# Performance work log

Measured on AMD Instinct MI355X. Metric: run time of the kernel, lower is better.

Reference implementation:

```python
import jax, jax.numpy as jnp
import numpy as np

N_NODES = 100000
N_EDGES = 1600000
D = 128        # in_dim == hidden_dim (forced by x_j + xe in message)
C = 64         # num_classes
G = 128        # number of graphs in the batch
BN_EPS = 1e-5


def setup_inputs() -> dict:
    key = jax.random.key(0)
    ks = jax.random.split(key, 14)
    s = 0.05
    inp = {
        "x": jax.random.normal(ks[0], (N_NODES, D), dtype=jnp.float32),
        "xe": jax.random.normal(ks[1], (N_EDGES, D), dtype=jnp.float32),
        "edge_index": jax.random.randint(ks[2], (2, N_EDGES), 0, N_NODES, dtype=jnp.int32),
        "batch": jnp.sort(jax.random.randint(ks[3], (N_NODES,), 0, G, dtype=jnp.int32)),
        # layer 0 MySAGEConv params
        "Wl0": jax.random.normal(ks[4], (D, D), dtype=jnp.float32) * s,
        "bl0": jnp.zeros((D,), dtype=jnp.float32),
        "Wr0": jax.random.normal(ks[5], (D, D), dtype=jnp.float32) * s,
        # layer 1 MySAGEConv params
        "Wl1": jax.random.normal(ks[6], (D, D), dtype=jnp.float32) * s,
        "bl1": jnp.zeros((D,), dtype=jnp.float32),
        "Wr1": jax.random.normal(ks[7], (D, D), dtype=jnp.float32) * s,
        # BatchNorm (only applied after non-final layers -> layer 0)
        "gamma0": jnp.ones((D,), dtype=jnp.float32),
        "beta0": jnp.zeros((D,), dtype=jnp.float32),
        # readout projection
        "Wp": jax.random.normal(ks[8], (C, D), dtype=jnp.float32) * s,
        "bp": jnp.zeros((C,), dtype=jnp.float32),
    }
    return inp


def _segment_mean(vals, idx, num_segments):
    s = jax.ops.segment_sum(vals, idx, num_segments=num_segments)
    cnt = jax.ops.segment_sum(jnp.ones((vals.shape[0],), vals.dtype), idx,
                              num_segments=num_segments)
    return s / jnp.clip(cnt, 1.0)[:, None]


def _my_sage_conv(h, xe, src, dst, Wl, bl, Wr):
    # message: relu(x_j + xe); aggregate: scatter-mean at dst; then lin_l + lin_r
    msg = jax.nn.relu(h[src] + xe)                       # [E, D]
    agg = _segment_mean(msg, dst, N_NODES)               # [N, D]
    return agg @ Wl.T + bl + h @ Wr.T


def _batchnorm_train(h, gamma, beta):
    mu = jnp.mean(h, axis=0)
    var = jnp.var(h, axis=0)
    return gamma * (h - mu) * jax.lax.rsqrt(var + BN_EPS) + beta


def reference(x, xe, edge_index, batch,
              Wl0, bl0, Wr0, Wl1, bl1, Wr1,
              gamma0, beta0, Wp, bp):
    src, dst = edge_index[0], edge_index[1]
    # layer 0: conv -> BN -> ReLU
    h = _my_sage_conv(x, xe, src, dst, Wl0, bl0, Wr0)
    h = jax.nn.relu(_batchnorm_train(h, gamma0, beta0))
    # layer 1 (last): conv only
    h = _my_sage_conv(h, xe, src, dst, Wl1, bl1, Wr1)
    # graph readout (global mean pool over pre-proj node features)
    g = _segment_mean(h, batch, G)                       # [G, D]
    # readout projection on nodes
    h = jax.nn.relu(h) @ Wp.T + bp                       # [N, C]
    return h, g
```

## Files before the change

kernel.cpp:

```cpp
#include <hip/hip_runtime.h>

#define N_NODES 100000
#define N_EDGES 1600000
#define DIM 128
#define NCLS 64
#define NG 128
#define BN_EPS 1e-5f

typedef __attribute__((ext_vector_type(8))) short s16x8;
typedef __attribute__((ext_vector_type(4))) float f32x4;
#define MFMA_BF16 __builtin_amdgcn_mfma_f32_16x16x32_bf16

__device__ __forceinline__ void f2hl8(float4 v0, float4 v1, s16x8& h8, s16x8& l8) {
    float vv[8] = {v0.x, v0.y, v0.z, v0.w, v1.x, v1.y, v1.z, v1.w};
#pragma unroll
    for (int i = 0; i < 8; ++i) {
        unsigned u = __float_as_uint(vv[i]);
        short h = (short)(u >> 16);
        float r = vv[i] - __uint_as_float(u & 0xFFFF0000u);
        short l = (short)(__float_as_uint(r) >> 16);
        h8[i] = h;
        l8[i] = l;
    }
}

__device__ __forceinline__ float4 relu4(float4 v) {
    v.x = fmaxf(v.x, 0.f); v.y = fmaxf(v.y, 0.f);
    v.z = fmaxf(v.z, 0.f); v.w = fmaxf(v.w, 0.f);
    return v;
}

__global__ void k_hist(const int* __restrict__ dst, int* __restrict__ cnt) {
    int e = blockIdx.x * 256 + threadIdx.x;
    if (e < N_EDGES) atomicAdd(&cnt[dst[e]], 1);
}

__global__ void k_scan1(const int* __restrict__ cnt, int* __restrict__ rowptr,
                        int* __restrict__ bsums) {
    __shared__ int sd[1024];
    int tid = threadIdx.x;
    int i = blockIdx.x * 1024 + tid;
    int v = (i < N_NODES) ? cnt[i] : 0;
    sd[tid] = v;
    __syncthreads();
    for (int off = 1; off < 1024; off <<= 1) {
        int t2 = (tid >= off) ? sd[tid - off] : 0;
        __syncthreads();
        sd[tid] += t2;
        __syncthreads();
    }
    if (i < N_NODES) rowptr[i] = sd[tid] - v;
    if (tid == 1023) bsums[blockIdx.x] = sd[tid];
}

__global__ void k_scan2(int* __restrict__ bsums, int nb) {
    __shared__ int sd[128];
    int t = threadIdx.x;
    int v = (t < nb) ? bsums[t] : 0;
    sd[t] = v;
    __syncthreads();
    for (int off = 1; off < 128; off <<= 1) {
        int u = (t >= off) ? sd[t - off] : 0;
        __syncthreads();
        sd[t] += u;
        __syncthreads();
    }
    if (t < nb) bsums[t] = sd[t] - v;
}

__global__ void k_scan3(int* __restrict__ rowptr, const int* __restrict__ bsums,
                        int* __restrict__ wcur) {
    int i = blockIdx.x * 1024 + threadIdx.x;
    if (i < N_NODES) {
        int v = rowptr[i] + bsums[blockIdx.x];
        rowptr[i] = v;
        wcur[i] = v;
    }
    if (i == N_NODES - 1) rowptr[N_NODES] = N_EDGES;
}

__global__ void k_scatter(const int* __restrict__ src, const int* __restrict__ dst,
                          int* __restrict__ wcur, int2* __restrict__ esort) {
    int e = blockIdx.x * 256 + threadIdx.x;
    if (e < N_EDGES) {
        int d = dst[e];
        int p = atomicAdd(&wcur[d], 1);
        esort[p] = make_int2(e, src[e]);
    }
}

__global__ __launch_bounds__(256) void k_agg(
        const float* __restrict__ F, const float* __restrict__ xe,
        const int* __restrict__ rowptr, const int2* __restrict__ esort,
        float* __restrict__ agg, const float* __restrict__ bnsc, int applyBN) {
    int wid = (blockIdx.x * blockDim.x + threadIdx.x) >> 6;
    int lane = threadIdx.x & 63;
    if (wid >= N_NODES) return;
    int half = lane >> 5;
    int l = lane & 31;
    int p0 = rowptr[wid], p1 = rowptr[wid + 1];
    if (p0 == p1) {
        if (half == 0) {
            float4 z = make_float4(0.f, 0.f, 0.f, 0.f);
            *reinterpret_cast<float4*>(&agg[(size_t)wid * DIM + l * 4]) = z;
        }
        return;
    }
    float4 sc, sh;
    if (applyBN) {
        sc = *reinterpret_cast<const float4*>(&bnsc[l * 4]);
        sh = *reinterpret_cast<const float4*>(&bnsc[DIM + l * 4]);
    }
    float4 acc = make_float4(0.f, 0.f, 0.f, 0.f);
    for (int p = p0; p < p1; p += 8) {
        int q0 = p + half;
        int q1 = p + 2 + half;
        int q2 = p + 4 + half;
        int q3 = p + 6 + half;
        int2 e0 = esort[min(q0, p1 - 1)];
        int2 e1 = esort[min(q1, p1 - 1)];
        int2 e2 = esort[min(q2, p1 - 1)];
        int2 e3 = esort[min(q3, p1 - 1)];
        float4 a0 = *reinterpret_cast<const float4*>(&F[(size_t)e0.y * DIM + l * 4]);
        float4 b0 = *reinterpret_cast<const float4*>(&xe[(size_t)e0.x * DIM + l * 4]);
        float4 a1 = *reinterpret_cast<const float4*>(&F[(size_t)e1.y * DIM + l * 4]);
        float4 b1 = *reinterpret_cast<const float4*>(&xe[(size_t)e1.x * DIM + l * 4]);
        float4 a2 = *reinterpret_cast<const float4*>(&F[(size_t)e2.y * DIM + l * 4]);
        float4 b2 = *reinterpret_cast<const float4*>(&xe[(size_t)e2.x * DIM + l * 4]);
        float4 a3 = *reinterpret_cast<const float4*>(&F[(size_t)e3.y * DIM + l * 4]);
        float4 b3 = *reinterpret_cast<const float4*>(&xe[(size_t)e3.x * DIM + l * 4]);
        if (applyBN) {
            a0.x = fmaxf(a0.x * sc.x + sh.x, 0.f); a0.y = fmaxf(a0.y * sc.y + sh.y, 0.f);
            a0.z = fmaxf(a0.z * sc.z + sh.z, 0.f); a0.w = fmaxf(a0.w * sc.w + sh.w, 0.f);
            a1.x = fmaxf(a1.x * sc.x + sh.x, 0.f); a1.y = fmaxf(a1.y * sc.y + sh.y, 0.f);
            a1.z = fmaxf(a1.z * sc.z + sh.z, 0.f); a1.w = fmaxf(a1.w * sc.w + sh.w, 0.f);
            a2.x = fmaxf(a2.x * sc.x + sh.x, 0.f); a2.y = fmaxf(a2.y * sc.y + sh.y, 0.f);
            a2.z = fmaxf(a2.z * sc.z + sh.z, 0.f); a2.w = fmaxf(a2.w * sc.w + sh.w, 0.f);
            a3.x = fmaxf(a3.x * sc.x + sh.x, 0.f); a3.y = fmaxf(a3.y * sc.y + sh.y, 0.f);
            a3.z = fmaxf(a3.z * sc.z + sh.z, 0.f); a3.w = fmaxf(a3.w * sc.w + sh.w, 0.f);
        }
        if (q0 < p1) {
            acc.x += fmaxf(a0.x + b0.x, 0.f); acc.y += fmaxf(a0.y + b0.y, 0.f);
            acc.z += fmaxf(a0.z + b0.z, 0.f); acc.w += fmaxf(a0.w + b0.w, 0.f);
        }
        if (q1 < p1) {
            acc.x += fmaxf(a1.x + b1.x, 0.f); acc.y += fmaxf(a1.y + b1.y, 0.f);
            acc.z += fmaxf(a1.z + b1.z, 0.f); acc.w += fmaxf(a1.w + b1.w, 0.f);
        }
        if (q2 < p1) {
            acc.x += fmaxf(a2.x + b2.x, 0.f); acc.y += fmaxf(a2.y + b2.y, 0.f);
            acc.z += fmaxf(a2.z + b2.z, 0.f); acc.w += fmaxf(a2.w + b2.w, 0.f);
        }
        if (q3 < p1) {
            acc.x += fmaxf(a3.x + b3.x, 0.f); acc.y += fmaxf(a3.y + b3.y, 0.f);
            acc.z += fmaxf(a3.z + b3.z, 0.f); acc.w += fmaxf(a3.w + b3.w, 0.f);
        }
    }
    acc.x += __shfl_xor(acc.x, 32);
    acc.y += __shfl_xor(acc.y, 32);
    acc.z += __shfl_xor(acc.z, 32);
    acc.w += __shfl_xor(acc.w, 32);
    if (half == 0) {
        float s = 1.f / (float)(p1 - p0);
        acc.x *= s; acc.y *= s; acc.z *= s; acc.w *= s;
        *reinterpret_cast<float4*>(&agg[(size_t)wid * DIM + l * 4]) = acc;
    }
}

__global__ void k_wprep_all(const float* __restrict__ Wl0, const float* __restrict__ Wr0,
                            const float* __restrict__ Wl1, const float* __restrict__ Wr1,
                            const float* __restrict__ Wp,
                            short* __restrict__ fWl0h, short* __restrict__ fWl0l,
                            short* __restrict__ fWr0h, short* __restrict__ fWr0l,
                            short* __restrict__ fWl1h, short* __restrict__ fWl1l,
                            short* __restrict__ fWr1h, short* __restrict__ fWr1l,
                            short* __restrict__ fWph, short* __restrict__ fWpl) {
    int b = blockIdx.x;
    const float* W; short* hi; short* lo; int ct;
    if (b < 8)       { W = Wl0; hi = fWl0h; lo = fWl0l; ct = b; }
    else if (b < 16) { W = Wr0; hi = fWr0h; lo = fWr0l; ct = b - 8; }
    else if (b < 24) { W = Wl1; hi = fWl1h; lo = fWl1l; ct = b - 16; }
    else if (b < 32) { W = Wr1; hi = fWr1h; lo = fWr1l; ct = b - 24; }
    else             { W = Wp;  hi = fWph;  lo = fWpl;  ct = b - 32; }
    int tt = threadIdx.x;
    int lane = tt & 63, ks = (tt >> 6) & 3;
    int row = ct * 16 + (lane & 15);
    int k0 = ks * 32 + ((lane >> 4) << 3);
    float4 v0 = *reinterpret_cast<const float4*>(&W[(size_t)row * DIM + k0]);
    float4 v1 = *reinterpret_cast<const float4*>(&W[(size_t)row * DIM + k0 + 4]);
    s16x8 h8, l8;
    f2hl8(v0, v1, h8, l8);
    int t = ct * 256 + ks * 64 + lane;
    *reinterpret_cast<s16x8*>(&hi[(size_t)t * 8]) = h8;
    *reinterpret_cast<s16x8*>(&lo[(size_t)t * 8]) = l8;
}

__global__ __launch_bounds__(256) void k_gemm2(
        const float* __restrict__ A, const float* __restrict__ B,
        const short* __restrict__ fW1h, const short* __restrict__ fW1l,
        const short* __restrict__ fW2h, const short* __restrict__ fW2l,
        const float* __restrict__ bias, float* __restrict__ OUT,
        float* __restrict__ bnacc, const float* __restrict__ bnsc,
        int doBN, int bnB) {
    int t = threadIdx.x, w = t >> 6, l = t & 63;
    int n0 = blockIdx.x * 128;
    int r = l & 15, kh = l >> 4;
    int row0 = n0 + w * 16 + r;
    int row1 = row0 + 64;
    int n_0 = min(row0, N_NODES - 1);
    int n_1 = min(row1, N_NODES - 1);

    f32x4 acc0[8], acc1[8];
#pragma unroll
    for (int ct = 0; ct < 8; ++ct) {
        acc0[ct] = (f32x4){0.f, 0.f, 0.f, 0.f};
        acc1[ct] = (f32x4){0.f, 0.f, 0.f, 0.f};
    }
    const s16x8* w1h = (const s16x8*)fW1h;
    const s16x8* w1l = (const s16x8*)fW1l;
    const s16x8* w2h = (const s16x8*)fW2h;
    const s16x8* w2l = (const s16x8*)fW2l;

#pragma unroll
    for (int ks = 0; ks < 4; ++ks) {
        int kb = ks * 32 + kh * 8;
        float4 va0 = *reinterpret_cast<const float4*>(&A[(size_t)n_0 * DIM + kb]);
        float4 va1 = *reinterpret_cast<const float4*>(&A[(size_t)n_0 * DIM + kb + 4]);
        float4 vb0 = *reinterpret_cast<const float4*>(&B[(size_t)n_0 * DIM + kb]);
        float4 vb1 = *reinterpret_cast<const float4*>(&B[(size_t)n_0 * DIM + kb + 4]);
        float4 wa0 = *reinterpret_cast<const float4*>(&A[(size_t)n_1 * DIM + kb]);
        float4 wa1 = *reinterpret_cast<const float4*>(&A[(size_t)n_1 * DIM + kb + 4]);
        float4 wb0 = *reinterpret_cast<const float4*>(&B[(size_t)n_1 * DIM + kb]);
        float4 wb1 = *reinterpret_cast<const float4*>(&B[(size_t)n_1 * DIM + kb + 4]);
        if (bnB) {
            float4 sc0 = *reinterpret_cast<const float4*>(&bnsc[kb]);
            float4 sh0 = *reinterpret_cast<const float4*>(&bnsc[DIM + kb]);
            float4 sc1 = *reinterpret_cast<const float4*>(&bnsc[kb + 4]);
            float4 sh1 = *reinterpret_cast<const float4*>(&bnsc[DIM + kb + 4]);
            vb0.x = fmaxf(vb0.x * sc0.x + sh0.x, 0.f);
            vb0.y = fmaxf(vb0.y * sc0.y + sh0.y, 0.f);
            vb0.z = fmaxf(vb0.z * sc0.z + sh0.z, 0.f);
            vb0.w = fmaxf(vb0.w * sc0.w + sh0.w, 0.f);
            vb1.x = fmaxf(vb1.x * sc1.x + sh1.x, 0.f);
            vb1.y = fmaxf(vb1.y * sc1.y + sh1.y, 0.f);
            vb1.z = fmaxf(vb1.z * sc1.z + sh1.z, 0.f);
            vb1.w = fmaxf(vb1.w * sc1.w + sh1.w, 0.f);
            wb0.x = fmaxf(wb0.x * sc0.x + sh0.x, 0.f);
            wb0.y = fmaxf(wb0.y * sc0.y + sh0.y, 0.f);
            wb0.z = fmaxf(wb0.z * sc0.z + sh0.z, 0.f);
            wb0.w = fmaxf(wb0.w * sc0.w + sh0.w, 0.f);
            wb1.x = fmaxf(wb1.x * sc1.x + sh1.x, 0.f);
            wb1.y = fmaxf(wb1.y * sc1.y + sh1.y, 0.f);
            wb1.z = fmaxf(wb1.z * sc1.z + sh1.z, 0.f);
            wb1.w = fmaxf(wb1.w * sc1.w + sh1.w, 0.f);
        }
        s16x8 a0h, a0l, b0h, b0l, a1h, a1l, b1h, b1l;
        f2hl8(va0, va1, a0h, a0l);
        f2hl8(vb0, vb1, b0h, b0l);
        f2hl8(wa0, wa1, a1h, a1l);
        f2hl8(wb0, wb1, b1h, b1l);
        int fb = ks * 64 + l;
#pragma unroll
        for (int ct = 0; ct < 8; ++ct) {
            int fi = ct * 256 + fb;
            s16x8 wh1 = w1h[fi], wl1 = w1l[fi];
            s16x8 wh2 = w2h[fi], wl2 = w2l[fi];
            acc0[ct] = MFMA_BF16(a0h, wh1, acc0[ct], 0, 0, 0);
            acc0[ct] = MFMA_BF16(a0h, wl1, acc0[ct], 0, 0, 0);
            acc0[ct] = MFMA_BF16(a0l, wh1, acc0[ct], 0, 0, 0);
            acc0[ct] = MFMA_BF16(b0h, wh2, acc0[ct], 0, 0, 0);
            acc0[ct] = MFMA_BF16(b0h, wl2, acc0[ct], 0, 0, 0);
            acc0[ct] = MFMA_BF16(b0l, wh2, acc0[ct], 0, 0, 0);
            acc1[ct] = MFMA_BF16(a1h, wh1, acc1[ct], 0, 0, 0);
            acc1[ct] = MFMA_BF16(a1h, wl1, acc1[ct], 0, 0, 0);
            acc1[ct] = MFMA_BF16(a1l, wh1, acc1[ct], 0, 0, 0);
            acc1[ct] = MFMA_BF16(b1h, wh2, acc1[ct], 0, 0, 0);
            acc1[ct] = MFMA_BF16(b1h, wl2, acc1[ct], 0, 0, 0);
            acc1[ct] = MFMA_BF16(b1l, wh2, acc1[ct], 0, 0, 0);
        }
    }

    float p1s[8], p2s[8];
    int col0 = l & 15;
    int nb0 = n0 + w * 16 + (kh << 2);
    int nb1 = nb0 + 64;
#pragma unroll
    for (int ct = 0; ct < 8; ++ct) {
        float bj = bias[ct * 16 + col0];
        float s1 = 0.f, s2 = 0.f;
#pragma unroll
        for (int rr = 0; rr < 4; ++rr) {
            int n = nb0 + rr;
            float h = acc0[ct][rr] + bj;
            if (n < N_NODES) {
                OUT[(size_t)n * DIM + ct * 16 + col0] = h;
                s1 += h; s2 += h * h;
            }
            n = nb1 + rr;
            h = acc1[ct][rr] + bj;
            if (n < N_NODES) {
                OUT[(size_t)n * DIM + ct * 16 + col0] = h;
                s1 += h; s2 += h * h;
            }
        }
        p1s[ct] = s1; p2s[ct] = s2;
    }
    if (doBN) {
        __shared__ float red1[512];
        __shared__ float red2[512];
#pragma unroll
        for (int ct = 0; ct < 8; ++ct) {
            p1s[ct] += __shfl_xor(p1s[ct], 16);
            p1s[ct] += __shfl_xor(p1s[ct], 32);
            p2s[ct] += __shfl_xor(p2s[ct], 16);
            p2s[ct] += __shfl_xor(p2s[ct], 32);
        }
        if (l < 16) {
#pragma unroll
            for (int ct = 0; ct < 8; ++ct) {
                red1[w * 128 + ct * 16 + l] = p1s[ct];
                red2[w * 128 + ct * 16 + l] = p2s[ct];
            }
        }
        __syncthreads();
        if (t < 128) {
            float s1 = red1[t] + red1[128 + t] + red1[256 + t] + red1[384 + t];
            float s2 = red2[t] + red2[128 + t] + red2[256 + t] + red2[384 + t];
            atomicAdd(&bnacc[t], s1);
            atomicAdd(&bnacc[128 + t], s2);
        }
    }
}

__global__ void k_bnfinal(const float* __restrict__ bnacc, const float* __restrict__ gamma,
                          const float* __restrict__ beta, float* __restrict__ bnsc) {
    int d = threadIdx.x;
    if (d < DIM) {
        float mu = bnacc[d] / (float)N_NODES;
        float var = bnacc[128 + d] / (float)N_NODES - mu * mu;
        float rstd = rsqrtf(var + BN_EPS);
        float sc = gamma[d] * rstd;
        bnsc[d] = sc;
        bnsc[128 + d] = beta[d] - mu * sc;
    }
}

__global__ void k_pool(const float* __restrict__ H1, const int* __restrict__ batch,
                       float* __restrict__ gout) {
    __shared__ float red[4][128];
    int g = blockIdx.x;
    int t = threadIdx.x;
    int d = t & 127;
    int sl = t >> 7;
    int lo = 0, hi = N_NODES;
    while (lo < hi) { int m = (lo + hi) >> 1; if (batch[m] < g) lo = m + 1; else hi = m; }
    int s = lo;
    lo = 0; hi = N_NODES;
    while (lo < hi) { int m = (lo + hi) >> 1; if (batch[m] < g + 1) lo = m + 1; else hi = m; }
    int e = lo;
    float sum = 0.f;
    for (int n = s + sl; n < e; n += 4) sum += H1[(size_t)n * DIM + d];
    red[sl][d] = sum;
    __syncthreads();
    if (t < 128) {
        float tot = red[0][d] + red[1][d] + red[2][d] + red[3][d];
        gout[g * DIM + d] = tot / (float)max(e - s, 1);
    }
}

__global__ __launch_bounds__(256) void k_proj(
        const float* __restrict__ H1, const short* __restrict__ fWph,
        const short* __restrict__ fWpl, const float* __restrict__ bp,
        float* __restrict__ OUT) {
    int t = threadIdx.x, w = t >> 6, l = t & 63;
    int n0 = blockIdx.x * 128;
    int r = l & 15, kh = l >> 4;
    int row0 = n0 + w * 16 + r;
    int row1 = row0 + 64;
    int n_0 = min(row0, N_NODES - 1);
    int n_1 = min(row1, N_NODES - 1);
    f32x4 acc0[4], acc1[4];
#pragma unroll
    for (int ct = 0; ct < 4; ++ct) {
        acc0[ct] = (f32x4){0.f, 0.f, 0.f, 0.f};
        acc1[ct] = (f32x4){0.f, 0.f, 0.f, 0.f};
    }
    const s16x8* wph = (const s16x8*)fWph;
    const s16x8* wpl = (const s16x8*)fWpl;
#pragma unroll
    for (int ks = 0; ks < 4; ++ks) {
        int kb = ks * 32 + kh * 8;
        float4 va0 = relu4(*reinterpret_cast<const float4*>(&H1[(size_t)n_0 * DIM + kb]));
        float4 va1 = relu4(*reinterpret_cast<const float4*>(&H1[(size_t)n_0 * DIM + kb + 4]));
        float4 wa0 = relu4(*reinterpret_cast<const float4*>(&H1[(size_t)n_1 * DIM + kb]));
        float4 wa1 = relu4(*reinterpret_cast<const float4*>(&H1[(size_t)n_1 * DIM + kb + 4]));
        s16x8 a0h, a0l, a1h, a1l;
        f2hl8(va0, va1, a0h, a0l);
        f2hl8(wa0, wa1, a1h, a1l);
        int fb = ks * 64 + l;
#pragma unroll
        for (int ct = 0; ct < 4; ++ct) {
            int fi = ct * 256 + fb;
            s16x8 wh = wph[fi], wl = wpl[fi];
            acc0[ct] = MFMA_BF16(a0h, wh, acc0[ct], 0, 0, 0);
            acc0[ct] = MFMA_BF16(a0h, wl, acc0[ct], 0, 0, 0);
            acc0[ct] = MFMA_BF16(a0l, wh, acc0[ct], 0, 0, 0);
            acc1[ct] = MFMA_BF16(a1h, wh, acc1[ct], 0, 0, 0);
            acc1[ct] = MFMA_BF16(a1h, wl, acc1[ct], 0, 0, 0);
            acc1[ct] = MFMA_BF16(a1l, wh, acc1[ct], 0, 0, 0);
        }
    }
    int col0 = l & 15;
    int nb0 = n0 + w * 16 + (kh << 2);
    int nb1 = nb0 + 64;
#pragma unroll
    for (int ct = 0; ct < 4; ++ct) {
        float bj = bp[ct * 16 + col0];
#pragma unroll
        for (int rr = 0; rr < 4; ++rr) {
            int n = nb0 + rr;
            if (n < N_NODES)
                OUT[(size_t)n * NCLS + ct * 16 + col0] = acc0[ct][rr] + bj;
            n = nb1 + rr;
            if (n < N_NODES)
                OUT[(size_t)n * NCLS + ct * 16 + col0] = acc1[ct][rr] + bj;
        }
    }
}

extern "C" void kernel_launch(void* const* d_in, const int* in_sizes, int n_in,
                              void* d_out, int out_size, void* d_ws, size_t ws_size,
                              hipStream_t stream) {
    (void)in_sizes; (void)n_in; (void)out_size; (void)ws_size;
    const float* x     = (const float*)d_in[0];
    const float* xe    = (const float*)d_in[1];
    const int*   eidx  = (const int*)d_in[2];
    const int*   batch = (const int*)d_in[3];
    const float* Wl0   = (const float*)d_in[4];
    const float* bl0   = (const float*)d_in[5];
    const float* Wr0   = (const float*)d_in[6];
    const float* Wl1   = (const float*)d_in[7];
    const float* bl1   = (const float*)d_in[8];
    const float* Wr1   = (const float*)d_in[9];
    const float* gamma0 = (const float*)d_in[10];
    const float* beta0  = (const float*)d_in[11];
    const float* Wp    = (const float*)d_in[12];
    const float* bp    = (const float*)d_in[13];
    const int* srcp = eidx;
    const int* dstp = eidx + N_EDGES;

    char* ws = (char*)d_ws;
    size_t off = 0;
    auto carve = [&](size_t bytes) {
        void* p = ws + off;
        off = (off + bytes + 255) & ~(size_t)255;
        return p;
    };
    int*   cnt    = (int*)carve((size_t)N_NODES * 4);
    int*   rowptr = (int*)carve((size_t)(N_NODES + 1) * 4);
    int*   wcur   = (int*)carve((size_t)N_NODES * 4);
    int*   bsums  = (int*)carve(128 * 4);
    float* bnacc  = (float*)carve(256 * 4);
    float* bnsc   = (float*)carve(256 * 4);
    int2*  esort  = (int2*)carve((size_t)N_EDGES * 8);
    float* AGG    = (float*)carve((size_t)N_NODES * DIM * 4);
    float* H      = (float*)carve((size_t)N_NODES * DIM * 4);
    float* H1     = (float*)carve((size_t)N_NODES * DIM * 4);
    short* fWl0h = (short*)carve(16384 * 2);
    short* fWl0l = (short*)carve(16384 * 2);
    short* fWr0h = (short*)carve(16384 * 2);
    short* fWr0l = (short*)carve(16384 * 2);
    short* fWl1h = (short*)carve(16384 * 2);
    short* fWl1l = (short*)carve(16384 * 2);
    short* fWr1h = (short*)carve(16384 * 2);
    short* fWr1l = (short*)carve(16384 * 2);
    short* fWph  = (short*)carve(8192 * 2);
    short* fWpl  = (short*)carve(8192 * 2);

    float* out_h = (float*)d_out;
    float* out_g = out_h + (size_t)N_NODES * NCLS;

    hipMemsetAsync(cnt, 0, (size_t)N_NODES * 4, stream);
    hipMemsetAsync(bnacc, 0, 256 * 4, stream);

    k_wprep_all<<<36, 256, 0, stream>>>(Wl0, Wr0, Wl1, Wr1, Wp,
                                        fWl0h, fWl0l, fWr0h, fWr0l,
                                        fWl1h, fWl1l, fWr1h, fWr1l,
                                        fWph, fWpl);

    int nb = (N_NODES + 1023) / 1024;
    k_hist<<<(N_EDGES + 255) / 256, 256, 0, stream>>>(dstp, cnt);
    k_scan1<<<nb, 1024, 0, stream>>>(cnt, rowptr, bsums);
    k_scan2<<<1, 128, 0, stream>>>(bsums, nb);
    k_scan3<<<nb, 1024, 0, stream>>>(rowptr, bsums, wcur);
    k_scatter<<<(N_EDGES + 255) / 256, 256, 0, stream>>>(srcp, dstp, wcur, esort);

    int gblocks = (N_NODES + 127) / 128;

    k_agg<<<(N_NODES * 64 + 255) / 256, 256, 0, stream>>>(x, xe, rowptr, esort, AGG,
                                                          bnsc, 0);
    k_gemm2<<<gblocks, 256, 0, stream>>>(AGG, x, fWl0h, fWl0l, fWr0h, fWr0l,
                                         bl0, H, bnacc, bnsc, 1, 0);
    k_bnfinal<<<1, 128, 0, stream>>>(bnacc, gamma0, beta0, bnsc);

    k_agg<<<(N_NODES * 64 + 255) / 256, 256, 0, stream>>>(H, xe, rowptr, esort, AGG,
                                                          bnsc, 1);
    k_gemm2<<<gblocks, 256, 0, stream>>>(AGG, H, fWl1h, fWl1l, fWr1h, fWr1l,
                                         bl1, H1, bnacc, bnsc, 0, 1);

    k_pool<<<NG, 512, 0, stream>>>(H1, batch, out_g);
    k_proj<<<gblocks, 256, 0, stream>>>(H1, fWph, fWpl, bp, out_h);
}
```

Baseline: 889.6 us.

## Store node features and edge features in bf16, pre-permuted xe by destination

Converts x and the layer-0 hidden state to bf16 so the gather in aggregation reads half the bytes. During the CSR scatter it also writes a bf16 copy of xe permuted into destination-sorted order, so aggregation reads xe sequentially instead of gathering it randomly. The GEMM's root-weight operand now uses a single bf16 term instead of a hi/lo split, which cuts MFMA count. The cost is lower precision in the gathered features, the hidden state and the root GEMM path, plus an extra 400MB write of sorted xe when the workspace allows it.

```diff
diff --git a/kernel.cpp b/kernel.cpp
--- a/kernel.cpp
+++ b/kernel.cpp
@@ -10,6 +10,19 @@
 typedef __attribute__((ext_vector_type(8))) short s16x8;
 typedef __attribute__((ext_vector_type(4))) float f32x4;
 #define MFMA_BF16 __builtin_amdgcn_mfma_f32_16x16x32_bf16
+
+__device__ __forceinline__ unsigned short f2b(float x) {
+    unsigned u = __float_as_uint(x);
+    return (unsigned short)((u + 0x7FFFu + ((u >> 16) & 1u)) >> 16);
+}
+__device__ __forceinline__ float b2f(unsigned short s) {
+    return __uint_as_float(((unsigned)s) << 16);
+}
+__device__ __forceinline__ float4 bexp4(ushort4 u) {
+    float4 f;
+    f.x = b2f(u.x); f.y = b2f(u.y); f.z = b2f(u.z); f.w = b2f(u.w);
+    return f;
+}
 
 __device__ __forceinline__ void f2hl8(float4 v0, float4 v1, s16x8& h8, s16x8& l8) {
     float vv[8] = {v0.x, v0.y, v0.z, v0.w, v1.x, v1.y, v1.z, v1.w};
@@ -28,6 +41,19 @@
     v.x = fmaxf(v.x, 0.f); v.y = fmaxf(v.y, 0.f);
     v.z = fmaxf(v.z, 0.f); v.w = fmaxf(v.w, 0.f);
     return v;
+}
+
+__global__ void k_cvt(const float* __restrict__ in, unsigned short* __restrict__ out,
+                      int n8) {
+    int i = blockIdx.x * 256 + threadIdx.x;
+    if (i >= n8) return;
+    float4 a = reinterpret_cast<const float4*>(in)[(size_t)i * 2];
+    float4 b = reinterpret_cast<const float4*>(in)[(size_t)i * 2 + 1];
+    ushort4 oa, ob;
+    oa.x = f2b(a.x); oa.y = f2b(a.y); oa.z = f2b(a.z); oa.w = f2b(a.w);
+    ob.x = f2b(b.x); ob.y = f2b(b.y); ob.z = f2b(b.z); ob.w = f2b(b.w);
+    reinterpret_cast<ushort4*>(out)[(size_t)i * 2] = oa;
+    reinterpret_cast<ushort4*>(out)[(size_t)i * 2 + 1] = ob;
 }
 
 __global__ void k_hist(const int* __restrict__ dst, int* __restrict__ cnt) {
@@ -79,21 +105,36 @@
     if (i == N_NODES - 1) rowptr[N_NODES] = N_EDGES;
 }
 
-__global__ void k_scatter(const int* __restrict__ src, const int* __restrict__ dst,
-                          int* __restrict__ wcur, int2* __restrict__ esort) {
-    int e = blockIdx.x * 256 + threadIdx.x;
-    if (e < N_EDGES) {
-        int d = dst[e];
-        int p = atomicAdd(&wcur[d], 1);
-        esort[p] = make_int2(e, src[e]);
-    }
-}
-
+template <int PACK>
+__global__ __launch_bounds__(256) void k_scatter(
+        const int* __restrict__ src, const int* __restrict__ dst,
+        int* __restrict__ wcur, int2* __restrict__ esort,
+        const float* __restrict__ xe, unsigned short* __restrict__ xe_s) {
+    int wid = (blockIdx.x * 256 + threadIdx.x) >> 6;
+    int lane = threadIdx.x & 63;
+    int half = lane >> 5, l = lane & 31;
+    long e = (long)wid * 2 + half;
+    if (e >= N_EDGES) return;
+    int s = src[e], d = dst[e];
+    int p0 = 0;
+    if (l == 0) p0 = atomicAdd(&wcur[d], 1);
+    int p = __shfl(p0, half * 32);
+    if (l == 0) esort[p] = make_int2((int)e, s);
+    if (PACK) {
+        float4 v = *reinterpret_cast<const float4*>(&xe[(size_t)e * DIM + l * 4]);
+        ushort4 o;
+        o.x = f2b(v.x); o.y = f2b(v.y); o.z = f2b(v.z); o.w = f2b(v.w);
+        *reinterpret_cast<ushort4*>(&xe_s[(size_t)p * DIM + l * 4]) = o;
+    }
+}
+
+template <int XES>
 __global__ __launch_bounds__(256) void k_agg(
-        const float* __restrict__ F, const float* __restrict__ xe,
+        const unsigned short* __restrict__ Fb, const float* __restrict__ xe,
+        const unsigned short* __restrict__ xe_s,
         const int* __restrict__ rowptr, const int2* __restrict__ esort,
         float* __restrict__ agg, const float* __restrict__ bnsc, int applyBN) {
-    int wid = (blockIdx.x * blockDim.x + threadIdx.x) >> 6;
+    int wid = (blockIdx.x * 256 + threadIdx.x) >> 6;
     int lane = threadIdx.x & 63;
     if (wid >= N_NODES) return;
     int half = lane >> 5;
@@ -113,47 +154,33 @@
     }
     float4 acc = make_float4(0.f, 0.f, 0.f, 0.f);
     for (int p = p0; p < p1; p += 8) {
-        int q0 = p + half;
-        int q1 = p + 2 + half;
-        int q2 = p + 4 + half;
-        int q3 = p + 6 + half;
-        int2 e0 = esort[min(q0, p1 - 1)];
-        int2 e1 = esort[min(q1, p1 - 1)];
-        int2 e2 = esort[min(q2, p1 - 1)];
-        int2 e3 = esort[min(q3, p1 - 1)];
-        float4 a0 = *reinterpret_cast<const float4*>(&F[(size_t)e0.y * DIM + l * 4]);
-        float4 b0 = *reinterpret_cast<const float4*>(&xe[(size_t)e0.x * DIM + l * 4]);
-        float4 a1 = *reinterpret_cast<const float4*>(&F[(size_t)e1.y * DIM + l * 4]);
-        float4 b1 = *reinterpret_cast<const float4*>(&xe[(size_t)e1.x * DIM + l * 4]);
-        float4 a2 = *reinterpret_cast<const float4*>(&F[(size_t)e2.y * DIM + l * 4]);
-        float4 b2 = *reinterpret_cast<const float4*>(&xe[(size_t)e2.x * DIM + l * 4]);
-        float4 a3 = *reinterpret_cast<const float4*>(&F[(size_t)e3.y * DIM + l * 4]);
-        float4 b3 = *reinterpret_cast<const float4*>(&xe[(size_t)e3.x * DIM + l * 4]);
-        if (applyBN) {
-            a0.x = fmaxf(a0.x * sc.x + sh.x, 0.f); a0.y = fmaxf(a0.y * sc.y + sh.y, 0.f);
-            a0.z = fmaxf(a0.z * sc.z + sh.z, 0.f); a0.w = fmaxf(a0.w * sc.w + sh.w, 0.f);
-            a1.x = fmaxf(a1.x * sc.x + sh.x, 0.f); a1.y = fmaxf(a1.y * sc.y + sh.y, 0.f);
-            a1.z = fmaxf(a1.z * sc.z + sh.z, 0.f); a1.w = fmaxf(a1.w * sc.w + sh.w, 0.f);
-            a2.x = fmaxf(a2.x * sc.x + sh.x, 0.f); a2.y = fmaxf(a2.y * sc.y + sh.y, 0.f);
-            a2.z = fmaxf(a2.z * sc.z + sh.z, 0.f); a2.w = fmaxf(a2.w * sc.w + sh.w, 0.f);
-            a3.x = fmaxf(a3.x * sc.x + sh.x, 0.f); a3.y = fmaxf(a3.y * sc.y + sh.y, 0.f);
-            a3.z = fmaxf(a3.z * sc.z + sh.z, 0.f); a3.w = fmaxf(a3.w * sc.w + sh.w, 0.f);
-        }
-        if (q0 < p1) {
-            acc.x += fmaxf(a0.x + b0.x, 0.f); acc.y += fmaxf(a0.y + b0.y, 0.f);
-            acc.z += fmaxf(a0.z + b0.z, 0.f); acc.w += fmaxf(a0.w + b0.w, 0.f);
-        }
-        if (q1 < p1) {
-            acc.x += fmaxf(a1.x + b1.x, 0.f); acc.y += fmaxf(a1.y + b1.y, 0.f);
-            acc.z += fmaxf(a1.z + b1.z, 0.f); acc.w += fmaxf(a1.w + b1.w, 0.f);
-        }
-        if (q2 < p1) {
-            acc.x += fmaxf(a2.x + b2.x, 0.f); acc.y += fmaxf(a2.y + b2.y, 0.f);
-            acc.z += fmaxf(a2.z + b2.z, 0.f); acc.w += fmaxf(a2.w + b2.w, 0.f);
-        }
-        if (q3 < p1) {
-            acc.x += fmaxf(a3.x + b3.x, 0.f); acc.y += fmaxf(a3.y + b3.y, 0.f);
-            acc.z += fmaxf(a3.z + b3.z, 0.f); acc.w += fmaxf(a3.w + b3.w, 0.f);
+#pragma unroll
+        for (int j = 0; j < 4; ++j) {
+            int q = p + j * 2 + half;
+            int qc = min(q, p1 - 1);
+            int2 es = esort[qc];
+            float4 a = bexp4(*reinterpret_cast<const ushort4*>(
+                &Fb[(size_t)es.y * DIM + l * 4]));
+            float4 b;
+            if (XES) {
+                b = bexp4(*reinterpret_cast<const ushort4*>(
+                    &xe_s[(size_t)qc * DIM + l * 4]));
+            } else {
+                b = *reinterpret_cast<const float4*>(
+                    &xe[(size_t)es.x * DIM + l * 4]);
+            }
+            if (applyBN) {
+                a.x = fmaxf(a.x * sc.x + sh.x, 0.f);
+                a.y = fmaxf(a.y * sc.y + sh.y, 0.f);
+                a.z = fmaxf(a.z * sc.z + sh.z, 0.f);
+                a.w = fmaxf(a.w * sc.w + sh.w, 0.f);
+            }
+            if (q < p1) {
+                acc.x += fmaxf(a.x + b.x, 0.f);
+                acc.y += fmaxf(a.y + b.y, 0.f);
+                acc.z += fmaxf(a.z + b.z, 0.f);
+                acc.w += fmaxf(a.w + b.w, 0.f);
+            }
         }
     }
     acc.x += __shfl_xor(acc.x, 32);
@@ -196,10 +223,11 @@
 }
 
 __global__ __launch_bounds__(256) void k_gemm2(
-        const float* __restrict__ A, const float* __restrict__ B,
+        const float* __restrict__ A, const unsigned short* __restrict__ Bbf,
         const short* __restrict__ fW1h, const short* __restrict__ fW1l,
         const short* __restrict__ fW2h, const short* __restrict__ fW2l,
-        const float* __restrict__ bias, float* __restrict__ OUT,
+        const float* __restrict__ bias, float* __restrict__ OUTf,
+        unsigned short* __restrict__ OUTb,
         float* __restrict__ bnacc, const float* __restrict__ bnsc,
         int doBN, int bnB) {
     int t = threadIdx.x, w = t >> 6, l = t & 63;
@@ -226,39 +254,28 @@
         int kb = ks * 32 + kh * 8;
         float4 va0 = *reinterpret_cast<const float4*>(&A[(size_t)n_0 * DIM + kb]);
         float4 va1 = *reinterpret_cast<const float4*>(&A[(size_t)n_0 * DIM + kb + 4]);
-        float4 vb0 = *reinterpret_cast<const float4*>(&B[(size_t)n_0 * DIM + kb]);
-        float4 vb1 = *reinterpret_cast<const float4*>(&B[(size_t)n_0 * DIM + kb + 4]);
         float4 wa0 = *reinterpret_cast<const float4*>(&A[(size_t)n_1 * DIM + kb]);
         float4 wa1 = *reinterpret_cast<const float4*>(&A[(size_t)n_1 * DIM + kb + 4]);
-        float4 wb0 = *reinterpret_cast<const float4*>(&B[(size_t)n_1 * DIM + kb]);
-        float4 wb1 = *reinterpret_cast<const float4*>(&B[(size_t)n_1 * DIM + kb + 4]);
+        s16x8 b0 = *reinterpret_cast<const s16x8*>(&Bbf[(size_t)n_0 * DIM + kb]);
+        s16x8 b1 = *reinterpret_cast<const s16x8*>(&Bbf[(size_t)n_1 * DIM + kb]);
         if (bnB) {
             float4 sc0 = *reinterpret_cast<const float4*>(&bnsc[kb]);
             float4 sh0 = *reinterpret_cast<const float4*>(&bnsc[DIM + kb]);
             float4 sc1 = *reinterpret_cast<const float4*>(&bnsc[kb + 4]);
             float4 sh1 = *reinterpret_cast<const float4*>(&bnsc[DIM + kb + 4]);
-            vb0.x = fmaxf(vb0.x * sc0.x + sh0.x, 0.f);
-            vb0.y = fmaxf(vb0.y * sc0.y + sh0.y, 0.f);
-            vb0.z = fmaxf(vb0.z * sc0.z + sh0.z, 0.f);
-            vb0.w = fmaxf(vb0.w * sc0.w + sh0.w, 0.f);
-            vb1.x = fmaxf(vb1.x * sc1.x + sh1.x, 0.f);
-            vb1.y = fmaxf(vb1.y * sc1.y + sh1.y, 0.f);
-            vb1.z = fmaxf(vb1.z * sc1.z + sh1.z, 0.f);
-            vb1.w = fmaxf(vb1.w * sc1.w + sh1.w, 0.f);
-            wb0.x = fmaxf(wb0.x * sc0.x + sh0.x, 0.f);
-            wb0.y = fmaxf(wb0.y * sc0.y + sh0.y, 0.f);
-            wb0.z = fmaxf(wb0.z * sc0.z + sh0.z, 0.f);
-            wb0.w = fmaxf(wb0.w * sc0.w + sh0.w, 0.f);
-            wb1.x = fmaxf(wb1.x * sc1.x + sh1.x, 0.f);
-            wb1.y = fmaxf(wb1.y * sc1.y + sh1.y, 0.f);
-            wb1.z = fmaxf(wb1.z * sc1.z + sh1.z, 0.f);
-            wb1.w = fmaxf(wb1.w * sc1.w + sh1.w, 0.f);
-        }
-        s16x8 a0h, a0l, b0h, b0l, a1h, a1l, b1h, b1l;
+            float scv[8] = {sc0.x, sc0.y, sc0.z, sc0.w, sc1.x, sc1.y, sc1.z, sc1.w};
+            float shv[8] = {sh0.x, sh0.y, sh0.z, sh0.w, sh1.x, sh1.y, sh1.z, sh1.w};
+#pragma unroll
+            for (int i = 0; i < 8; ++i) {
+                float v = b2f((unsigned short)b0[i]);
+                b0[i] = (short)f2b(fmaxf(v * scv[i] + shv[i], 0.f));
+                v = b2f((unsigned short)b1[i]);
+                b1[i] = (short)f2b(fmaxf(v * scv[i] + shv[i], 0.f));
+            }
+        }
+        s16x8 a0h, a0l, a1h, a1l;
         f2hl8(va0, va1, a0h, a0l);
-        f2hl8(vb0, vb1, b0h, b0l);
         f2hl8(wa0, wa1, a1h, a1l);
-        f2hl8(wb0, wb1, b1h, b1l);
         int fb = ks * 64 + l;
 #pragma unroll
         for (int ct = 0; ct < 8; ++ct) {
@@ -268,15 +285,13 @@
             acc0[ct] = MFMA_BF16(a0h, wh1, acc0[ct], 0, 0, 0);
             acc0[ct] = MFMA_BF16(a0h, wl1, acc0[ct], 0, 0, 0);
             acc0[ct] = MFMA_BF16(a0l, wh1, acc0[ct], 0, 0, 0);
-            acc0[ct] = MFMA_BF16(b0h, wh2, acc0[ct], 0, 0, 0);
-            acc0[ct] = MFMA_BF16(b0h, wl2, acc0[ct], 0, 0, 0);
-            acc0[ct] = MFMA_BF16(b0l, wh2, acc0[ct], 0, 0, 0);
+            acc0[ct] = MFMA_BF16(b0, wh2, acc0[ct], 0, 0, 0);
+            acc0[ct] = MFMA_BF16(b0, wl2, acc0[ct], 0, 0, 0);
             acc1[ct] = MFMA_BF16(a1h, wh1, acc1[ct], 0, 0, 0);
             acc1[ct] = MFMA_BF16(a1h, wl1, acc1[ct], 0, 0, 0);
             acc1[ct] = MFMA_BF16(a1l, wh1, acc1[ct], 0, 0, 0);
-            acc1[ct] = MFMA_BF16(b1h, wh2, acc1[ct], 0, 0, 0);
-            acc1[ct] = MFMA_BF16(b1h, wl2, acc1[ct], 0, 0, 0);
-            acc1[ct] = MFMA_BF16(b1l, wh2, acc1[ct], 0, 0, 0);
+            acc1[ct] = MFMA_BF16(b1, wh2, acc1[ct], 0, 0, 0);
+            acc1[ct] = MFMA_BF16(b1, wl2, acc1[ct], 0, 0, 0);
         }
     }
 
@@ -293,13 +308,15 @@
             int n = nb0 + rr;
             float h = acc0[ct][rr] + bj;
             if (n < N_NODES) {
-                OUT[(size_t)n * DIM + ct * 16 + col0] = h;
+                if (OUTb) OUTb[(size_t)n * DIM + ct * 16 + col0] = f2b(h);
+                else      OUTf[(size_t)n * DIM + ct * 16 + col0] = h;
                 s1 += h; s2 += h * h;
             }
             n = nb1 + rr;
             h = acc1[ct][rr] + bj;
             if (n < N_NODES) {
-                OUT[(size_t)n * DIM + ct * 16 + col0] = h;
+                if (OUTb) OUTb[(size_t)n * DIM + ct * 16 + col0] = f2b(h);
+                else      OUTf[(size_t)n * DIM + ct * 16 + col0] = h;
                 s1 += h; s2 += h * h;
             }
         }
@@ -431,7 +448,7 @@
 extern "C" void kernel_launch(void* const* d_in, const int* in_sizes, int n_in,
                               void* d_out, int out_size, void* d_ws, size_t ws_size,
                               hipStream_t stream) {
-    (void)in_sizes; (void)n_in; (void)out_size; (void)ws_size;
+    (void)in_sizes; (void)n_in; (void)out_size;
     const float* x     = (const float*)d_in[0];
     const float* xe    = (const float*)d_in[1];
     const int*   eidx  = (const int*)d_in[2];
@@ -464,8 +481,9 @@
     float* bnsc   = (float*)carve(256 * 4);
     int2*  esort  = (int2*)carve((size_t)N_EDGES * 8);
     float* AGG    = (float*)carve((size_t)N_NODES * DIM * 4);
-    float* H      = (float*)carve((size_t)N_NODES * DIM * 4);
     float* H1     = (float*)carve((size_t)N_NODES * DIM * 4);
+    unsigned short* x_bf = (unsigned short*)carve((size_t)N_NODES * DIM * 2);
+    unsigned short* H_bf = (unsigned short*)carve((size_t)N_NODES * DIM * 2);
     short* fWl0h = (short*)carve(16384 * 2);
     short* fWl0l = (short*)carve(16384 * 2);
     short* fWr0h = (short*)carve(16384 * 2);
@@ -477,6 +495,10 @@
     short* fWph  = (short*)carve(8192 * 2);
     short* fWpl  = (short*)carve(8192 * 2);
 
+    size_t xes_bytes = (size_t)N_EDGES * DIM * 2;
+    int pack = (off + xes_bytes + 256 <= ws_size) ? 1 : 0;
+    unsigned short* xe_s = pack ? (unsigned short*)carve(xes_bytes) : nullptr;
+
     float* out_h = (float*)d_out;
     float* out_g = out_h + (size_t)N_NODES * NCLS;
 
@@ -487,26 +509,36 @@
                                         fWl0h, fWl0l, fWr0h, fWr0l,
                                         fWl1h, fWl1l, fWr1h, fWr1l,
                                         fWph, fWpl);
+    k_cvt<<<(N_NODES * DIM / 8 + 255) / 256, 256, 0, stream>>>(x, x_bf,
+                                                               N_NODES * DIM / 8);
 
     int nb = (N_NODES + 1023) / 1024;
     k_hist<<<(N_EDGES + 255) / 256, 256, 0, stream>>>(dstp, cnt);
     k_scan1<<<nb, 1024, 0, stream>>>(cnt, rowptr, bsums);
     k_scan2<<<1, 128, 0, stream>>>(bsums, nb);
     k_scan3<<<nb, 1024, 0, stream>>>(rowptr, bsums, wcur);
-    k_scatter<<<(N_EDGES + 255) / 256, 256, 0, stream>>>(srcp, dstp, wcur, esort);
-
+    if (pack)
+        k_scatter<1><<<N_EDGES / 8, 256, 0, stream>>>(srcp, dstp, wcur, esort, xe, xe_s);
+    else
+        k_scatter<0><<<N_EDGES / 8, 256, 0, stream>>>(srcp, dstp, wcur, esort, xe, nullptr);
+
+    int ablocks = (N_NODES * 64 + 255) / 256;
     int gblocks = (N_NODES + 127) / 128;
 
-    k_agg<<<(N_NODES * 64 + 255) / 256, 256, 0, stream>>>(x, xe, rowptr, esort, AGG,
-                                                          bnsc, 0);
-    k_gemm2<<<gblocks, 256, 0, stream>>>(AGG, x, fWl0h, fWl0l, fWr0h, fWr0l,
-                                         bl0, H, bnacc, bnsc, 1, 0);
+    if (pack)
+        k_agg<1><<<ablocks, 256, 0, stream>>>(x_bf, xe, xe_s, rowptr, esort, AGG, bnsc, 0);
+    else
+        k_agg<0><<<ablocks, 256, 0, stream>>>(x_bf, xe, nullptr, rowptr, esort, AGG, bnsc, 0);
+    k_gemm2<<<gblocks, 256, 0, stream>>>(AGG, x_bf, fWl0h, fWl0l, fWr0h, fWr0l,
+                                         bl0, nullptr, H_bf, bnacc, bnsc, 1, 0);
     k_bnfinal<<<1, 128, 0, stream>>>(bnacc, gamma0, beta0, bnsc);
 
-    k_agg<<<(N_NODES * 64 + 255) / 256, 256, 0, stream>>>(H, xe, rowptr, esort, AGG,
-                                                          bnsc, 1);
-    k_gemm2<<<gblocks, 256, 0, stream>>>(AGG, H, fWl1h, fWl1l, fWr1h, fWr1l,
-                                         bl1, H1, bnacc, bnsc, 0, 1);
+    if (pack)
+        k_agg<1><<<ablocks, 256, 0, stream>>>(H_bf, xe, xe_s, rowptr, esort, AGG, bnsc, 1);
+    else
+        k_agg<0><<<ablocks, 256, 0, stream>>>(H_bf, xe, nullptr, rowptr, esort, AGG, bnsc, 1);
+    k_gemm2<<<gblocks, 256, 0, stream>>>(AGG, H_bf, fWl1h, fWl1l, fWr1h, fWr1l,
+                                         bl1, H1, nullptr, bnacc, bnsc, 0, 1);
 
     k_pool<<<NG, 512, 0, stream>>>(H1, batch, out_g);
     k_proj<<<gblocks, 256, 0, stream>>>(H1, fWph, fWpl, bp, out_h);
```

New measurement: 945.7 us. 6.3% more time.
